# Kernel optimization log

Hardware: AMD Instinct MI355X
Metric: run time of the kernel (lower is better)

The kernel has to match this reference:

```python
import jax, jax.numpy as jnp
import numpy as np

EPS = 1e-5
PC_LO = jnp.array([-51.2, -51.2, -5.0], dtype=jnp.float32)
PC_HI = jnp.array([51.2, 51.2, 3.0], dtype=jnp.float32)
IMG_H, IMG_W = 256, 704
G, P = 1, 4  # num_groups, num_points


def _conv3x3(x, w, b):
    # x: NHWC, w: HWIO
    y = jax.lax.conv_general_dilated(x, w, (1, 1), 'SAME',
                                     dimension_numbers=('NHWC', 'HWIO', 'NHWC'))
    return y + b


def _inorm(x, eps=1e-5):
    # InstanceNorm2d (no affine), stats over H,W per (b,c); x NHWC
    m = jnp.mean(x, axis=(1, 2), keepdims=True)
    v = jnp.var(x, axis=(1, 2), keepdims=True)
    return (x - m) * jax.lax.rsqrt(v + eps)


def _bilinear(img, grid):
    # img [Hf,Wf,C], grid [...,2] in [-1,1]; align_corners=False, zero padding
    Hf, Wf, _ = img.shape
    x = (grid[..., 0] + 1.0) * 0.5 * Wf - 0.5
    y = (grid[..., 1] + 1.0) * 0.5 * Hf - 0.5
    x0 = jnp.floor(x)
    y0 = jnp.floor(y)

    def gather(xi, yi):
        inb = (xi >= 0) & (xi <= Wf - 1) & (yi >= 0) & (yi <= Hf - 1)
        v = img[jnp.clip(yi, 0, Hf - 1).astype(jnp.int32),
                jnp.clip(xi, 0, Wf - 1).astype(jnp.int32)]
        return v * inb[..., None].astype(img.dtype)

    wx1 = x - x0
    wy1 = y - y0
    wx0 = 1.0 - wx1
    wy0 = 1.0 - wy1
    return (gather(x0, y0) * (wx0 * wy0)[..., None]
            + gather(x0 + 1.0, y0) * (wx1 * wy0)[..., None]
            + gather(x0, y0 + 1.0) * (wx0 * wy1)[..., None]
            + gather(x0 + 1.0, y0 + 1.0) * (wx1 * wy1)[..., None])


def setup_inputs() -> dict:
    key = jax.random.key(0)
    ks = jax.random.split(key, 12)
    b, n, C = 1, 6, 128
    Hf, Wf = 32, 88
    Hb, Wb = 128, 128
    return {
        'mlvl_feats': jax.random.normal(ks[0], (b * n, C, Hf, Wf), jnp.float32),
        'lidar2img': jax.random.normal(ks[1], (b, n, 4, 4), jnp.float32),
        'bev_query': jax.random.normal(ks[2], (b, C, Hb, Wb), jnp.float32),
        'bev_pos': jax.random.uniform(ks[3], (b, Hb, Wb, 3), jnp.float32),
        'in_conv_w': jax.random.normal(ks[4], (3, 3, C, C), jnp.float32) * 0.02,
        'in_conv_b': jnp.zeros((C,), jnp.float32),
        'off_w': jax.random.normal(ks[5], (G * P * 3, C), jnp.float32) * 0.02,
        'off_b': jax.random.normal(ks[6], (G * P * 3,), jnp.float32),
        'mid_w1': jax.random.normal(ks[7], (512, 128 * P), jnp.float32) * 0.02,
        'mid_b1': jnp.zeros((512,), jnp.float32),
        'mid_w2': jax.random.normal(ks[8], (512, 512), jnp.float32) * 0.02,
        'mid_b2': jnp.zeros((512,), jnp.float32),
        'mid_w3': jax.random.normal(ks[9], (C, 512), jnp.float32) * 0.02,
        'mid_b3': jnp.zeros((C,), jnp.float32),
        'out_conv_w': jax.random.normal(ks[10], (3, 3, C, C), jnp.float32) * 0.02,
        'out_conv_b': jnp.zeros((C,), jnp.float32),
    }


def reference(mlvl_feats, lidar2img, bev_query, bev_pos, in_conv_w, in_conv_b,
              off_w, off_b, mid_w1, mid_b1, mid_w2, mid_b2, mid_w3, mid_b3,
              out_conv_w, out_conv_b):
    b, C, Hb, Wb = bev_query.shape
    n = lidar2img.shape[1]
    Q = Hb * Wb

    q = jnp.transpose(bev_query, (0, 2, 3, 1))  # NHWC [b,Hb,Wb,C]
    q = q + _conv3x3(q, in_conv_w, in_conv_b)
    q = _inorm(q)

    # --- SegSampling: predict offsets (1x1 conv + sigmoid), build 3D points ---
    off = jax.nn.sigmoid(jnp.einsum('bhwc,oc->bhwo', q, off_w) + off_b)
    off = off.reshape(b, Q, G, P, 3)  # 'b (g p d) h w -> b (h w) g p d'
    off_xy = off[..., :2] * (0.25 + EPS) * 2.0 - (0.25 + EPS)
    off_z = off[..., 2:3] * (4.0 + EPS) * 2.0 - (4.0 + EPS)
    ref = bev_pos.reshape(b, Q, 1, 1, 3) * (PC_HI - PC_LO) + PC_LO
    pts = ref + jnp.concatenate([off_xy, off_z], axis=-1)  # [b,Q,G,P,3]

    # --- project into each camera (sampling_4d) ---
    pts_h = jnp.concatenate([pts, jnp.ones_like(pts[..., :1])], axis=-1)
    cam = jnp.einsum('bnij,bqgpj->bnqgpi', lidar2img, pts_h)  # [b,n,Q,G,P,4]
    homo = cam[..., 2:3]
    uv = cam[..., :2] / jnp.maximum(homo, EPS)
    uv = uv / jnp.array([IMG_W, IMG_H], jnp.float32)  # normalized [0,1]
    valid = ((homo > EPS)
             & (uv[..., 0:1] > 0.0) & (uv[..., 0:1] < 1.0)
             & (uv[..., 1:2] > 0.0) & (uv[..., 1:2] < 1.0)).astype(q.dtype)
    grid = uv * 2.0 - 1.0  # [-1,1] for grid_sample

    # feats: [(b n), C, h, w] -> [b*n, h, w, C] (g=1)
    feat = jnp.transpose(mlvl_feats, (0, 2, 3, 1))
    grid_bn = grid.reshape(b * n, Q * G * P, 2)
    sampled = jax.vmap(_bilinear)(feat, grid_bn)  # [b*n, Q*G*P, C]
    sampled = sampled.reshape(b, n, Q, G, P, C)
    sampled = jnp.sum(sampled * valid, axis=1)  # mask-weighted sum over cameras

    # --- mid_conv: 1x1 conv MLP on (g p c) channels ---
    x = sampled.reshape(b, Hb, Wb, G * P * C)
    x = jax.nn.gelu(jnp.einsum('bhwi,oi->bhwo', x, mid_w1) + mid_b1, approximate=False)
    x = jax.nn.gelu(jnp.einsum('bhwi,oi->bhwo', x, mid_w2) + mid_b2, approximate=False)
    x = jnp.einsum('bhwi,oi->bhwo', x, mid_w3) + mid_b3
    q = _inorm(q + x)
    q = _inorm(q + _conv3x3(q, out_conv_w, out_conv_b))
    return jnp.transpose(q, (0, 3, 1, 2))  # back to NCHW
```

## Files before the change

kernel.cpp:

```cpp
#include <hip/hip_runtime.h>
#include <math.h>

#define QPIX 16384

typedef __bf16 bf16x8 __attribute__((ext_vector_type(8)));
typedef float f32x4 __attribute__((ext_vector_type(4)));

__device__ __forceinline__ unsigned short f2b(float f) {
  unsigned int x = __float_as_uint(f);
  unsigned int r = (x + 0x7fff + ((x >> 16) & 1)) >> 16;
  return (unsigned short)r;
}
__device__ __forceinline__ float b2f(unsigned short u) {
  return __uint_as_float(((unsigned int)u) << 16);
}

__device__ __forceinline__ void gld_lds16(const void* g, void* l) {
  __builtin_amdgcn_global_load_lds((__attribute__((address_space(1))) void*)(g),
                                   (__attribute__((address_space(3))) void*)(l), 16, 0, 0);
}

__device__ __forceinline__ int swz(int row, int ebase) {
  return row * 64 + ((((ebase) >> 3) ^ (row & 7)) << 3);
}

__global__ __launch_bounds__(256) void k_cvt_all(
    const float* __restrict__ feats, const float* __restrict__ bevq,
    const float* __restrict__ w1, const float* __restrict__ w2,
    const float* __restrict__ w3, const float* __restrict__ wo,
    const float* __restrict__ wi, unsigned short* __restrict__ featTb,
    unsigned short* __restrict__ qhi, unsigned short* __restrict__ qlo,
    unsigned short* __restrict__ w1b, unsigned short* __restrict__ w2b,
    unsigned short* __restrict__ w3b, unsigned short* __restrict__ wob,
    unsigned short* __restrict__ wibh, unsigned short* __restrict__ wibl,
    float* __restrict__ zerof) {
  __shared__ float tile[128][33];
  const int b = blockIdx.x, t = threadIdx.x;
  if (b == 0 && t < 160) zerof[t] = 0.f;
  if (b < 528) {
    const int img = b / 88;
    const int pb = (b - img * 88) * 32;
    const int p = t & 31, cg = t >> 5;
#pragma unroll
    for (int ci = 0; ci < 16; ++ci) {
      const int c = cg * 16 + ci;
      tile[c][p] = feats[((size_t)img * 128 + c) * 2816 + pb + p];
    }
    __syncthreads();
    const int c2 = t & 127, pw = t >> 7;
#pragma unroll
    for (int pp = pw; pp < 32; pp += 2)
      featTb[(size_t)img * 2816 * 128 + (size_t)(pb + pp) * 128 + c2] = f2b(tile[c2][pp]);
  } else if (b < 1040) {
    const int pb = (b - 528) * 32;
    const int p = t & 31, cg = t >> 5;
#pragma unroll
    for (int ci = 0; ci < 16; ++ci) {
      const int c = cg * 16 + ci;
      tile[c][p] = bevq[(size_t)c * QPIX + pb + p];
    }
    __syncthreads();
    const int c2 = t & 127, pw = t >> 7;
#pragma unroll
    for (int pp = pw; pp < 32; pp += 2) {
      float v = tile[c2][pp];
      unsigned short h = f2b(v);
      qhi[(size_t)(pb + pp) * 128 + c2] = h;
      qlo[(size_t)(pb + pp) * 128 + c2] = f2b(v - b2f(h));
    }
  } else {
    const int bb = b - 1040;
    if (bb < 1024) {
      int i = bb * 256 + t;
      w1b[i] = f2b(w1[i]);
    } else if (bb < 2048) {
      int i = (bb - 1024) * 256 + t;
      w2b[i] = f2b(w2[i]);
    } else if (bb < 2304) {
      int i = (bb - 2048) * 256 + t;
      w3b[i] = f2b(w3[i]);
    } else if (bb < 2880) {
      int i = (bb - 2304) * 256 + t;
      int n = i & 127, kk = i >> 7;
      int tap = kk >> 7, ci = kk & 127;
      wob[(size_t)n * 1152 + kk] = f2b(wo[(size_t)tap * 16384 + ci * 128 + n]);
    } else {
      int i = (bb - 2880) * 256 + t;
      int n = i & 127, kk = i >> 7;
      int tap = kk >> 7, ci = kk & 127;
      float v = wi[(size_t)tap * 16384 + ci * 128 + n];
      unsigned short h = f2b(v);
      wibh[(size_t)n * 1152 + kk] = h;
      wibl[(size_t)n * 1152 + kk] = f2b(v - b2f(h));
    }
  }
}

template <int BM, int BN, int MODE, int ACT, int RES, int OBF, int STATS>
__global__ __launch_bounds__(256) void mfma_gemm(
    const unsigned short* __restrict__ A, const unsigned short* __restrict__ A2,
    const unsigned short* __restrict__ Wt, const unsigned short* __restrict__ Wt2,
    const float* __restrict__ bias, const float* __restrict__ resid,
    const float* __restrict__ mrres, void* __restrict__ Out,
    float* __restrict__ partial, int N, int K,
    const unsigned short* __restrict__ zbuf) {
  constexpr int MI = BM / 32;
  constexpr int NJ = BN / 32;
  __shared__ unsigned short As[BM * 64];
  __shared__ unsigned short Bs[BN * 64];
  __shared__ unsigned short As2[(MODE == 2) ? BM * 64 : 1];
  __shared__ unsigned short Bs2[(MODE == 2) ? BN * 64 : 1];
  __shared__ float sred[STATS ? (BM / 8) : 1][STATS ? BN : 1];
  __shared__ float ssred[STATS ? (BM / 8) : 1][STATS ? BN : 1];

  const int t = threadIdx.x;
  const int lane = t & 63, w = t >> 6;
  const int wr = w >> 1, wc = w & 1;
  const int n0 = blockIdx.x * BN;
  const int m0 = blockIdx.y * BM;

  const int lrow = lane >> 3;
  const int akk = (((lane & 7) ^ (lrow & 7))) * 8;
  const int arow_l = wr * (BM / 2) + (lane & 15);
  const int brow_l = wc * (BN / 2) + (lane & 15);
  const int klane = (lane >> 4) * 8;

  f32x4 acc[MI][NJ];
#pragma unroll
  for (int i = 0; i < MI; ++i)
#pragma unroll
    for (int j = 0; j < NJ; ++j) acc[i][j] = (f32x4){0.f, 0.f, 0.f, 0.f};

  for (int k0 = 0; k0 < K; k0 += 64) {
#pragma unroll
    for (int q = 0; q < BM / 32; ++q) {
      const int r0 = w * (BM / 4) + q * 8;
      const int arow = r0 + lrow;
      const unsigned short* asrc;
      const unsigned short* asrc2 = zbuf;
      if (MODE == 0) {
        asrc = A + (size_t)(m0 + arow) * K + k0 + akk;
      } else {
        const int tap = k0 >> 7;
        const int dy = tap / 3 - 1, dx = tap % 3 - 1;
        const int pix = m0 + arow;
        const int hs = (pix >> 7) + dy;
        const int xs = (pix & 127) + dx;
        const bool ok = (hs >= 0) && (hs < 128) && (xs >= 0) && (xs < 128);
        const size_t srcoff = (size_t)((hs << 7) | (xs & 127)) * 128 + (k0 & 127) + akk;
        asrc = ok ? A + srcoff : zbuf;
        if (MODE == 2) asrc2 = ok ? A2 + srcoff : zbuf;
      }
      gld_lds16(asrc, &As[r0 * 64]);
      if (MODE == 2) gld_lds16(asrc2, &As2[r0 * 64]);
    }
#pragma unroll
    for (int q = 0; q < BN / 32; ++q) {
      const int r0 = w * (BN / 4) + q * 8;
      const int brow = r0 + lrow;
      gld_lds16(Wt + (size_t)(n0 + brow) * K + k0 + akk, &Bs[r0 * 64]);
      if (MODE == 2)
        gld_lds16(Wt2 + (size_t)(n0 + brow) * K + k0 + akk, &Bs2[r0 * 64]);
    }
    __syncthreads();
#pragma unroll
    for (int ks = 0; ks < 64; ks += 32) {
      bf16x8 af[MI], bfv[NJ];
#pragma unroll
      for (int i = 0; i < MI; ++i)
        af[i] = *(const bf16x8*)&As[swz(arow_l + i * 16, ks + klane)];
#pragma unroll
      for (int j = 0; j < NJ; ++j)
        bfv[j] = *(const bf16x8*)&Bs[swz(brow_l + j * 16, ks + klane)];
#pragma unroll
      for (int i = 0; i < MI; ++i)
#pragma unroll
        for (int j = 0; j < NJ; ++j)
          acc[i][j] = __builtin_amdgcn_mfma_f32_16x16x32_bf16(af[i], bfv[j], acc[i][j], 0, 0, 0);
      if (MODE == 2) {
        bf16x8 af2[MI], bf2[NJ];
#pragma unroll
        for (int i = 0; i < MI; ++i)
          af2[i] = *(const bf16x8*)&As2[swz(arow_l + i * 16, ks + klane)];
#pragma unroll
        for (int j = 0; j < NJ; ++j)
          bf2[j] = *(const bf16x8*)&Bs2[swz(brow_l + j * 16, ks + klane)];
#pragma unroll
        for (int i = 0; i < MI; ++i)
#pragma unroll
          for (int j = 0; j < NJ; ++j) {
            acc[i][j] = __builtin_amdgcn_mfma_f32_16x16x32_bf16(af[i], bf2[j], acc[i][j], 0, 0, 0);
            acc[i][j] = __builtin_amdgcn_mfma_f32_16x16x32_bf16(af2[i], bfv[j], acc[i][j], 0, 0, 0);
          }
      }
    }
    __syncthreads();
  }
  float sj[NJ], ssj[NJ];
#pragma unroll
  for (int j = 0; j < NJ; ++j) { sj[j] = 0.f; ssj[j] = 0.f; }
#pragma unroll
  for (int i = 0; i < MI; ++i) {
    const int mrow = m0 + wr * (BM / 2) + i * 16 + (lane >> 4) * 4;
#pragma unroll
    for (int j = 0; j < NJ; ++j) {
      const int col = n0 + wc * (BN / 2) + j * 16 + (lane & 15);
      const float bz = bias[col];
#pragma unroll
      for (int r = 0; r < 4; ++r) {
        const int m = mrow + r;
        float v = acc[i][j][r] + bz;
        if (RES == 1) v += resid[(size_t)m * 128 + col];
        if (RES == 2) v += resid[(size_t)col * QPIX + m];
        if (RES == 3)
          v += (resid[(size_t)m * 128 + col] - mrres[col]) * mrres[128 + col];
        if (ACT == 1) v = 0.5f * v * (1.f + erff(v * 0.70710678118654752f));
        if (OBF)
          ((unsigned short*)Out)[(size_t)m * N + col] = f2b(v);
        else
          ((float*)Out)[(size_t)m * N + col] = v;
        if (STATS) {
          sj[j] += v;
          ssj[j] += v * v;
        }
      }
    }
  }
  if (STATS) {
    const int cidx = wr * 4 + (lane >> 4);
#pragma unroll
    for (int j = 0; j < NJ; ++j) {
      const int cl = wc * (BN / 2) + j * 16 + (lane & 15);
      sred[cidx][cl] = sj[j];
      ssred[cidx][cl] = ssj[j];
    }
    __syncthreads();
    if (t < BN) {
      float s = 0.f, ss = 0.f;
#pragma unroll
      for (int kk = 0; kk < BM / 8; ++kk) {
        s += sred[kk][t];
        ss += ssred[kk][t];
      }
      partial[(size_t)(n0 + t) * 256 + blockIdx.y] = s;
      partial[32768 + (size_t)(n0 + t) * 256 + blockIdx.y] = ss;
    }
  }
}

__global__ __launch_bounds__(256) void k_stats_final(const float* __restrict__ partial,
                                                     float* __restrict__ mr) {
  __shared__ float s1[256], s2[256];
  const int c = blockIdx.x;
  const int t = threadIdx.x;
  s1[t] = partial[(size_t)c * 256 + t];
  s2[t] = partial[32768 + (size_t)c * 256 + t];
  __syncthreads();
#pragma unroll
  for (int off = 128; off > 0; off >>= 1) {
    if (t < off) {
      s1[t] += s1[t + off];
      s2[t] += s2[t + off];
    }
    __syncthreads();
  }
  if (t == 0) {
    float m = s1[0] * (1.f / 16384.f);
    float var = s2[0] * (1.f / 16384.f) - m * m;
    mr[c] = m;
    mr[128 + c] = rsqrtf(var + 1e-5f);
  }
}

__global__ __launch_bounds__(256) void k_offsets(
    const float* __restrict__ tB, const float* __restrict__ mr,
    const float* __restrict__ offw, const float* __restrict__ offb,
    const float* __restrict__ bpos, const float* __restrict__ l2i,
    float* __restrict__ pw, int* __restrict__ pidx) {
  __shared__ float ldsq[128 * 130];
  __shared__ float wT[128 * 12];
  __shared__ float bl[12];
  __shared__ float ml[128], rl[128];
  __shared__ float offl[128 * 12];
  __shared__ float Ll[96];
  const int t = threadIdx.x;
  const int qb = blockIdx.x * 128;
  for (int i = t; i < 1536; i += 256) wT[(i & 127) * 12 + (i >> 7)] = offw[i];
  if (t < 12) bl[t] = offb[t];
  if (t < 96) Ll[t] = l2i[t];
  if (t < 128) {
    ml[t] = mr[t];
    rl[t] = mr[128 + t];
  }
  __syncthreads();
#pragma unroll
  for (int j = 0; j < 32; ++j) {
    const int e = j * 512 + t * 2;
    const int c0 = e & 127;
    float2 v = *(const float2*)&tB[(size_t)qb * 128 + e];
    v.x = (v.x - ml[c0]) * rl[c0];
    v.y = (v.y - ml[c0 + 1]) * rl[c0 + 1];
    *(float2*)&ldsq[(e >> 7) * 130 + c0] = v;
  }
  __syncthreads();
  {
    const int qlc = t & 127, oh = t >> 7;
    float acc6[6];
#pragma unroll
    for (int o = 0; o < 6; ++o) acc6[o] = bl[oh * 6 + o];
    for (int c = 0; c < 128; ++c) {
      float qv = ldsq[qlc * 130 + c];
#pragma unroll
      for (int o = 0; o < 6; ++o) acc6[o] += qv * wT[c * 12 + oh * 6 + o];
    }
#pragma unroll
    for (int o = 0; o < 6; ++o)
      offl[qlc * 12 + oh * 6 + o] = 1.f / (1.f + expf(-acc6[o]));
  }
  __syncthreads();
  const float EPSf = 1e-5f;
#pragma unroll
  for (int ii = 0; ii < 12; ++ii) {
    const int item = ii * 256 + t;
    const int ql = item / 24;
    const int j = item - ql * 24;
    const int p = j / 6, n = j - p * 6;
    const int q = qb + ql;
    float o0 = offl[ql * 12 + p * 3 + 0];
    float o1 = offl[ql * 12 + p * 3 + 1];
    float o2 = offl[ql * 12 + p * 3 + 2];
    float ox = o0 * ((0.25f + EPSf) * 2.f) - (0.25f + EPSf);
    float oy = o1 * ((0.25f + EPSf) * 2.f) - (0.25f + EPSf);
    float oz = o2 * ((4.f + EPSf) * 2.f) - (4.f + EPSf);
    float px = bpos[q * 3 + 0] * 102.4f - 51.2f + ox;
    float py = bpos[q * 3 + 1] * 102.4f - 51.2f + oy;
    float pz = bpos[q * 3 + 2] * 8.f - 5.f + oz;
    const float* L = Ll + n * 16;
    float c0 = L[0] * px + L[1] * py + L[2] * pz + L[3];
    float c1 = L[4] * px + L[5] * py + L[6] * pz + L[7];
    float c2 = L[8] * px + L[9] * py + L[10] * pz + L[11];
    float d = fmaxf(c2, EPSf);
    float u = (c0 / d) / 704.f;
    float v = (c1 / d) / 256.f;
    float valid = (c2 > EPSf && u > 0.f && u < 1.f && v > 0.f && v < 1.f) ? 1.f : 0.f;
    float x = u * 88.f - 0.5f;
    float y = v * 32.f - 0.5f;
    float x0 = floorf(x), y0 = floorf(y);
    float wx1 = x - x0, wy1 = y - y0;
    float wx0 = 1.f - wx1, wy0 = 1.f - wy1;
    float4 wv;
    int4 iv;
    float* wvp = (float*)&wv;
    int* ivp = (int*)&iv;
#pragma unroll
    for (int k = 0; k < 4; ++k) {
      float xf = x0 + (float)(k & 1);
      float yf = y0 + (float)(k >> 1);
      bool inb = (xf >= 0.f) && (xf <= 87.f) && (yf >= 0.f) && (yf <= 31.f);
      float xc = fminf(fmaxf(xf, 0.f), 87.f);
      float yc = fminf(fmaxf(yf, 0.f), 31.f);
      ivp[k] = ((n * 32 + (int)yc) * 88 + (int)xc) * 128;
      float wgt = ((k & 1) ? wx1 : wx0) * ((k >> 1) ? wy1 : wy0);
      wvp[k] = inb ? wgt * valid : 0.f;
    }
    const size_t gi = (size_t)qb * 24 + item;
    *(float4*)&pw[gi * 4] = wv;
    *(int4*)&pidx[gi * 4] = iv;
  }
}

__global__ __launch_bounds__(256) void k_gather(const float* __restrict__ pw,
                                                const int* __restrict__ pidx,
                                                const unsigned short* __restrict__ featT,
                                                unsigned short* __restrict__ sampled) {
  const int q = blockIdx.x;
  const int t = threadIdx.x;
  const int p = t >> 6;
  const int lane = t & 63;
  const int half = lane >> 5, quad = lane & 31;
  float s0 = 0.f, s1 = 0.f, s2 = 0.f, s3 = 0.f;
#pragma unroll
  for (int cc = 0; cc < 3; ++cc) {
    const int n = half * 3 + cc;
    const size_t e = (size_t)(q * 24 + p * 6 + n) * 4;
    const float4 wv = *(const float4*)&pw[e];
    if (wv.x + wv.y + wv.z + wv.w != 0.f) {
      const int4 iv = *(const int4*)&pidx[e];
      ushort4 v0 = *(const ushort4*)&featT[(size_t)iv.x + quad * 4];
      ushort4 v1 = *(const ushort4*)&featT[(size_t)iv.y + quad * 4];
      ushort4 v2 = *(const ushort4*)&featT[(size_t)iv.z + quad * 4];
      ushort4 v3 = *(const ushort4*)&featT[(size_t)iv.w + quad * 4];
      s0 += wv.x * b2f(v0.x) + wv.y * b2f(v1.x) + wv.z * b2f(v2.x) + wv.w * b2f(v3.x);
      s1 += wv.x * b2f(v0.y) + wv.y * b2f(v1.y) + wv.z * b2f(v2.y) + wv.w * b2f(v3.y);
      s2 += wv.x * b2f(v0.z) + wv.y * b2f(v1.z) + wv.z * b2f(v2.z) + wv.w * b2f(v3.z);
      s3 += wv.x * b2f(v0.w) + wv.y * b2f(v1.w) + wv.z * b2f(v2.w) + wv.w * b2f(v3.w);
    }
  }
  s0 += __shfl_xor(s0, 32);
  s1 += __shfl_xor(s1, 32);
  s2 += __shfl_xor(s2, 32);
  s3 += __shfl_xor(s3, 32);
  if (half == 0) {
    ushort4 o;
    o.x = f2b(s0);
    o.y = f2b(s1);
    o.z = f2b(s2);
    o.w = f2b(s3);
    *(ushort4*)&sampled[(size_t)q * 512 + p * 128 + quad * 4] = o;
  }
}

__global__ __launch_bounds__(256) void k_apply2(const float* __restrict__ a,
                                                const float* __restrict__ mr,
                                                unsigned short* __restrict__ outb) {
  const size_t i = (size_t)blockIdx.x * 256 + threadIdx.x;
  const int c = (int)(i & 127);
  outb[i] = f2b((a[i] - mr[c]) * mr[128 + c]);
}

__global__ __launch_bounds__(256) void k_apply_t(const float* __restrict__ a,
                                                 const float* __restrict__ mr,
                                                 float* __restrict__ out) {
  __shared__ float tile[128][33];
  __shared__ float ml[128], rl[128];
  const int t = threadIdx.x;
  const int pb = blockIdx.x * 32;
  if (t < 128) {
    ml[t] = mr[t];
    rl[t] = mr[128 + t];
  }
  __syncthreads();
#pragma unroll
  for (int j = 0; j < 16; ++j) {
    const int e = j * 256 + t;
    const int pl = e >> 7, c = e & 127;
    const size_t gi = (size_t)(pb + pl) * 128 + c;
    tile[c][pl] = (a[gi] - ml[c]) * rl[c];
  }
  __syncthreads();
  const int p = t & 31, cb = t >> 5;
#pragma unroll
  for (int j = 0; j < 16; ++j) {
    const int c = cb + j * 8;
    out[(size_t)c * QPIX + pb + p] = tile[c][p];
  }
}

extern "C" void kernel_launch(void* const* d_in, const int* in_sizes, int n_in,
                              void* d_out, int out_size, void* d_ws, size_t ws_size,
                              hipStream_t stream) {
  const float* feats = (const float*)d_in[0];
  const float* l2i   = (const float*)d_in[1];
  const float* bevq  = (const float*)d_in[2];
  const float* bpos  = (const float*)d_in[3];
  const float* w_in  = (const float*)d_in[4];
  const float* b_in  = (const float*)d_in[5];
  const float* offw  = (const float*)d_in[6];
  const float* offb  = (const float*)d_in[7];
  const float* w1    = (const float*)d_in[8];
  const float* b1    = (const float*)d_in[9];
  const float* w2    = (const float*)d_in[10];
  const float* b2    = (const float*)d_in[11];
  const float* w3    = (const float*)d_in[12];
  const float* b3    = (const float*)d_in[13];
  const float* w_out = (const float*)d_in[14];
  const float* b_out = (const float*)d_in[15];
  float* out = (float*)d_out;

  const size_t QC = (size_t)QPIX * 128;
  float* ws = (float*)d_ws;
  float* tA = ws;
  float* tBb = tA + QC;
  float* partial = tBb + QC;
  float* mr1 = partial + 65536;
  float* mr2 = mr1 + 256;
  float* mr3 = mr2 + 256;
  float* zerof = mr3 + 256;
  float* pw = zerof + 160;
  int* pidx = (int*)(pw + 1572864);
  unsigned short* us = (unsigned short*)(pidx + 1572864);
  unsigned short* S1b = us;
  unsigned short* S2b = S1b + 8388608;
  unsigned short* featTb = S2b + 8388608;
  unsigned short* qhi = featTb + 2162688;
  unsigned short* qlo = qhi + 2097152;
  unsigned short* w1b = qlo + 2097152;
  unsigned short* w2b = w1b + 262144;
  unsigned short* w3b = w2b + 262144;
  unsigned short* wob = w3b + 65536;
  unsigned short* wibh = wob + 147456;
  unsigned short* wibl = wibh + 147456;
  const unsigned short* zb = (const unsigned short*)zerof;

  dim3 blk(256);

  k_cvt_all<<<4496, blk, 0, stream>>>(feats, bevq, w1, w2, w3, w_out, w_in,
                                      featTb, qhi, qlo, w1b, w2b, w3b, wob, wibh,
                                      wibl, zerof);

  mfma_gemm<64, 64, 2, 0, 2, 0, 1><<<dim3(2, 256), blk, 0, stream>>>(
      qhi, qlo, wibh, wibl, b_in, bevq, nullptr, tA, partial, 128, 1152, zb);
  k_stats_final<<<128, blk, 0, stream>>>(partial, mr1);

  k_offsets<<<128, blk, 0, stream>>>(tA, mr1, offw, offb, bpos, l2i, pw, pidx);

  k_gather<<<QPIX, blk, 0, stream>>>(pw, pidx, featTb, S1b);

  mfma_gemm<128, 128, 0, 1, 0, 1, 0><<<dim3(4, 128), blk, 0, stream>>>(
      S1b, nullptr, w1b, nullptr, b1, nullptr, nullptr, S2b, nullptr, 512, 512, zb);
  mfma_gemm<128, 128, 0, 1, 0, 1, 0><<<dim3(4, 128), blk, 0, stream>>>(
      S2b, nullptr, w2b, nullptr, b2, nullptr, nullptr, S1b, nullptr, 512, 512, zb);
  mfma_gemm<64, 64, 0, 0, 3, 0, 1><<<dim3(2, 256), blk, 0, stream>>>(
      S1b, nullptr, w3b, nullptr, b3, tA, mr1, tBb, partial, 128, 512, zb);
  k_stats_final<<<128, blk, 0, stream>>>(partial, mr2);
  k_apply2<<<8192, blk, 0, stream>>>(tBb, mr2, qhi);

  mfma_gemm<64, 64, 1, 0, 3, 0, 1><<<dim3(2, 256), blk, 0, stream>>>(
      qhi, nullptr, wob, nullptr, b_out, tBb, mr2, tA, partial, 128, 1152, zb);
  k_stats_final<<<128, blk, 0, stream>>>(partial, mr3);
  k_apply_t<<<512, blk, 0, stream>>>(tA, mr3, out);
}
```

Baseline: 161.6 us.

## Fuse stats finalization into GEMMs and merge offset and gather kernels

Removes the three separate stats-final kernels by having the last GEMM block (detected via an atomic counter) reduce the per-block partial sums and write the mean and rstd. Merges the offset computation and the bilinear gather into one kernel that keeps weights and indices in LDS, so the pw/pidx buffers no longer round-trip through global memory. The gather now uses 16-byte loads per lane, and k_apply2 is vectorized to float4. This cuts launches and global traffic, at the cost of a serial 256-row reduction in one block and reliance on counters being zeroed every call.

Result: slower. 347.7 us (+115.2%).

```diff
diff --git a/kernel.cpp b/kernel.cpp
--- a/kernel.cpp
+++ b/kernel.cpp
@@ -5,6 +5,7 @@
 
 typedef __bf16 bf16x8 __attribute__((ext_vector_type(8)));
 typedef float f32x4 __attribute__((ext_vector_type(4)));
+typedef unsigned short ushort8v __attribute__((ext_vector_type(8)));
 
 __device__ __forceinline__ unsigned short f2b(float f) {
   unsigned int x = __float_as_uint(f);
@@ -36,7 +37,7 @@
     float* __restrict__ zerof) {
   __shared__ float tile[128][33];
   const int b = blockIdx.x, t = threadIdx.x;
-  if (b == 0 && t < 160) zerof[t] = 0.f;
+  if (b == 0 && t < 176) zerof[t] = 0.f;
   if (b < 528) {
     const int img = b / 88;
     const int pb = (b - img * 88) * 32;
@@ -102,7 +103,8 @@
     const unsigned short* __restrict__ Wt, const unsigned short* __restrict__ Wt2,
     const float* __restrict__ bias, const float* __restrict__ resid,
     const float* __restrict__ mrres, void* __restrict__ Out,
-    float* __restrict__ partial, int N, int K,
+    float* __restrict__ partial, unsigned* __restrict__ cnt,
+    float* __restrict__ mrout, int N, int K,
     const unsigned short* __restrict__ zbuf) {
   constexpr int MI = BM / 32;
   constexpr int NJ = BN / 32;
@@ -112,6 +114,7 @@
   __shared__ unsigned short Bs2[(MODE == 2) ? BN * 64 : 1];
   __shared__ float sred[STATS ? (BM / 8) : 1][STATS ? BN : 1];
   __shared__ float ssred[STATS ? (BM / 8) : 1][STATS ? BN : 1];
+  __shared__ unsigned lastv;
 
   const int t = threadIdx.x;
   const int lane = t & 63, w = t >> 6;
@@ -242,49 +245,47 @@
         s += sred[kk][t];
         ss += ssred[kk][t];
       }
-      partial[(size_t)(n0 + t) * 256 + blockIdx.y] = s;
-      partial[32768 + (size_t)(n0 + t) * 256 + blockIdx.y] = ss;
-    }
-  }
-}
-
-__global__ __launch_bounds__(256) void k_stats_final(const float* __restrict__ partial,
-                                                     float* __restrict__ mr) {
-  __shared__ float s1[256], s2[256];
-  const int c = blockIdx.x;
-  const int t = threadIdx.x;
-  s1[t] = partial[(size_t)c * 256 + t];
-  s2[t] = partial[32768 + (size_t)c * 256 + t];
-  __syncthreads();
-#pragma unroll
-  for (int off = 128; off > 0; off >>= 1) {
-    if (t < off) {
-      s1[t] += s1[t + off];
-      s2[t] += s2[t + off];
-    }
-    __syncthreads();
-  }
-  if (t == 0) {
-    float m = s1[0] * (1.f / 16384.f);
-    float var = s2[0] * (1.f / 16384.f) - m * m;
-    mr[c] = m;
-    mr[128 + c] = rsqrtf(var + 1e-5f);
-  }
-}
-
-__global__ __launch_bounds__(256) void k_offsets(
+      partial[(size_t)blockIdx.y * 128 + n0 + t] = s;
+      partial[32768 + (size_t)blockIdx.y * 128 + n0 + t] = ss;
+    }
+    __threadfence();
+    __syncthreads();
+    if (t == 0) lastv = atomicAdd(cnt, 1u);
+    __syncthreads();
+    if (lastv == gridDim.x * gridDim.y - 1) {
+      __threadfence();
+      if (t < 128) {
+        float s = 0.f, ss = 0.f;
+#pragma unroll 4
+        for (int y = 0; y < 256; ++y) {
+          s += partial[(size_t)y * 128 + t];
+          ss += partial[32768 + (size_t)y * 128 + t];
+        }
+        float m = s * (1.f / 16384.f);
+        float var = ss * (1.f / 16384.f) - m * m;
+        mrout[t] = m;
+        mrout[128 + t] = rsqrtf(var + 1e-5f);
+      }
+    }
+  }
+}
+
+__global__ __launch_bounds__(256) void k_offgather(
     const float* __restrict__ tB, const float* __restrict__ mr,
     const float* __restrict__ offw, const float* __restrict__ offb,
     const float* __restrict__ bpos, const float* __restrict__ l2i,
-    float* __restrict__ pw, int* __restrict__ pidx) {
-  __shared__ float ldsq[128 * 130];
+    const unsigned short* __restrict__ featT,
+    unsigned short* __restrict__ sampled) {
   __shared__ float wT[128 * 12];
   __shared__ float bl[12];
+  __shared__ float Ll[96];
   __shared__ float ml[128], rl[128];
-  __shared__ float offl[128 * 12];
-  __shared__ float Ll[96];
+  __shared__ float ldsq[16 * 130];
+  __shared__ float offl[16 * 12];
+  __shared__ float cw[16 * 24 * 4];
+  __shared__ int cidx[16 * 24 * 4];
   const int t = threadIdx.x;
-  const int qb = blockIdx.x * 128;
+  const int qb = blockIdx.x * 16;
   for (int i = t; i < 1536; i += 256) wT[(i & 127) * 12 + (i >> 7)] = offw[i];
   if (t < 12) bl[t] = offb[t];
   if (t < 96) Ll[t] = l2i[t];
@@ -292,130 +293,106 @@
     ml[t] = mr[t];
     rl[t] = mr[128 + t];
   }
-  __syncthreads();
-#pragma unroll
-  for (int j = 0; j < 32; ++j) {
-    const int e = j * 512 + t * 2;
-    const int c0 = e & 127;
-    float2 v = *(const float2*)&tB[(size_t)qb * 128 + e];
-    v.x = (v.x - ml[c0]) * rl[c0];
-    v.y = (v.y - ml[c0 + 1]) * rl[c0 + 1];
-    *(float2*)&ldsq[(e >> 7) * 130 + c0] = v;
-  }
+  float4 ra = *(const float4*)&tB[(size_t)qb * 128 + t * 8];
+  float4 rb = *(const float4*)&tB[(size_t)qb * 128 + t * 8 + 4];
   __syncthreads();
   {
-    const int qlc = t & 127, oh = t >> 7;
-    float acc6[6];
-#pragma unroll
-    for (int o = 0; o < 6; ++o) acc6[o] = bl[oh * 6 + o];
-    for (int c = 0; c < 128; ++c) {
-      float qv = ldsq[qlc * 130 + c];
-#pragma unroll
-      for (int o = 0; o < 6; ++o) acc6[o] += qv * wT[c * 12 + oh * 6 + o];
-    }
-#pragma unroll
-    for (int o = 0; o < 6; ++o)
-      offl[qlc * 12 + oh * 6 + o] = 1.f / (1.f + expf(-acc6[o]));
+    const int e = t * 8;
+    const int q = e >> 7, c0 = e & 127;
+    float* d = &ldsq[q * 130 + c0];
+    const float va[8] = {ra.x, ra.y, ra.z, ra.w, rb.x, rb.y, rb.z, rb.w};
+#pragma unroll
+    for (int u = 0; u < 8; ++u) d[u] = (va[u] - ml[c0 + u]) * rl[c0 + u];
+  }
+  __syncthreads();
+  if (t < 192) {
+    const int q = t / 12, o = t - (t / 12) * 12;
+    float acc = bl[o];
+    for (int c = 0; c < 128; ++c) acc += ldsq[q * 130 + c] * wT[c * 12 + o];
+    offl[q * 12 + o] = 1.f / (1.f + expf(-acc));
   }
   __syncthreads();
   const float EPSf = 1e-5f;
 #pragma unroll
-  for (int ii = 0; ii < 12; ++ii) {
+  for (int ii = 0; ii < 2; ++ii) {
     const int item = ii * 256 + t;
-    const int ql = item / 24;
-    const int j = item - ql * 24;
-    const int p = j / 6, n = j - p * 6;
-    const int q = qb + ql;
-    float o0 = offl[ql * 12 + p * 3 + 0];
-    float o1 = offl[ql * 12 + p * 3 + 1];
-    float o2 = offl[ql * 12 + p * 3 + 2];
-    float ox = o0 * ((0.25f + EPSf) * 2.f) - (0.25f + EPSf);
-    float oy = o1 * ((0.25f + EPSf) * 2.f) - (0.25f + EPSf);
-    float oz = o2 * ((4.f + EPSf) * 2.f) - (4.f + EPSf);
-    float px = bpos[q * 3 + 0] * 102.4f - 51.2f + ox;
-    float py = bpos[q * 3 + 1] * 102.4f - 51.2f + oy;
-    float pz = bpos[q * 3 + 2] * 8.f - 5.f + oz;
-    const float* L = Ll + n * 16;
-    float c0 = L[0] * px + L[1] * py + L[2] * pz + L[3];
-    float c1 = L[4] * px + L[5] * py + L[6] * pz + L[7];
-    float c2 = L[8] * px + L[9] * py + L[10] * pz + L[11];
-    float d = fmaxf(c2, EPSf);
-    float u = (c0 / d) / 704.f;
-    float v = (c1 / d) / 256.f;
-    float valid = (c2 > EPSf && u > 0.f && u < 1.f && v > 0.f && v < 1.f) ? 1.f : 0.f;
-    float x = u * 88.f - 0.5f;
-    float y = v * 32.f - 0.5f;
-    float x0 = floorf(x), y0 = floorf(y);
-    float wx1 = x - x0, wy1 = y - y0;
-    float wx0 = 1.f - wx1, wy0 = 1.f - wy1;
-    float4 wv;
-    int4 iv;
-    float* wvp = (float*)&wv;
-    int* ivp = (int*)&iv;
-#pragma unroll
-    for (int k = 0; k < 4; ++k) {
-      float xf = x0 + (float)(k & 1);
-      float yf = y0 + (float)(k >> 1);
-      bool inb = (xf >= 0.f) && (xf <= 87.f) && (yf >= 0.f) && (yf <= 31.f);
-      float xc = fminf(fmaxf(xf, 0.f), 87.f);
-      float yc = fminf(fmaxf(yf, 0.f), 31.f);
-      ivp[k] = ((n * 32 + (int)yc) * 88 + (int)xc) * 128;
-      float wgt = ((k & 1) ? wx1 : wx0) * ((k >> 1) ? wy1 : wy0);
-      wvp[k] = inb ? wgt * valid : 0.f;
-    }
-    const size_t gi = (size_t)qb * 24 + item;
-    *(float4*)&pw[gi * 4] = wv;
-    *(int4*)&pidx[gi * 4] = iv;
-  }
-}
-
-__global__ __launch_bounds__(256) void k_gather(const float* __restrict__ pw,
-                                                const int* __restrict__ pidx,
-                                                const unsigned short* __restrict__ featT,
-                                                unsigned short* __restrict__ sampled) {
-  const int q = blockIdx.x;
-  const int t = threadIdx.x;
-  const int p = t >> 6;
-  const int lane = t & 63;
-  const int half = lane >> 5, quad = lane & 31;
-  float s0 = 0.f, s1 = 0.f, s2 = 0.f, s3 = 0.f;
-#pragma unroll
-  for (int cc = 0; cc < 3; ++cc) {
-    const int n = half * 3 + cc;
-    const size_t e = (size_t)(q * 24 + p * 6 + n) * 4;
-    const float4 wv = *(const float4*)&pw[e];
-    if (wv.x + wv.y + wv.z + wv.w != 0.f) {
-      const int4 iv = *(const int4*)&pidx[e];
-      ushort4 v0 = *(const ushort4*)&featT[(size_t)iv.x + quad * 4];
-      ushort4 v1 = *(const ushort4*)&featT[(size_t)iv.y + quad * 4];
-      ushort4 v2 = *(const ushort4*)&featT[(size_t)iv.z + quad * 4];
-      ushort4 v3 = *(const ushort4*)&featT[(size_t)iv.w + quad * 4];
-      s0 += wv.x * b2f(v0.x) + wv.y * b2f(v1.x) + wv.z * b2f(v2.x) + wv.w * b2f(v3.x);
-      s1 += wv.x * b2f(v0.y) + wv.y * b2f(v1.y) + wv.z * b2f(v2.y) + wv.w * b2f(v3.y);
-      s2 += wv.x * b2f(v0.z) + wv.y * b2f(v1.z) + wv.z * b2f(v2.z) + wv.w * b2f(v3.z);
-      s3 += wv.x * b2f(v0.w) + wv.y * b2f(v1.w) + wv.z * b2f(v2.w) + wv.w * b2f(v3.w);
-    }
-  }
-  s0 += __shfl_xor(s0, 32);
-  s1 += __shfl_xor(s1, 32);
-  s2 += __shfl_xor(s2, 32);
-  s3 += __shfl_xor(s3, 32);
-  if (half == 0) {
-    ushort4 o;
-    o.x = f2b(s0);
-    o.y = f2b(s1);
-    o.z = f2b(s2);
-    o.w = f2b(s3);
-    *(ushort4*)&sampled[(size_t)q * 512 + p * 128 + quad * 4] = o;
+    if (item < 384) {
+      const int ql = item / 24;
+      const int j = item - ql * 24;
+      const int p = j / 6, n = j - p * 6;
+      const int q = qb + ql;
+      float o0 = offl[ql * 12 + p * 3 + 0];
+      float o1 = offl[ql * 12 + p * 3 + 1];
+      float o2 = offl[ql * 12 + p * 3 + 2];
+      float ox = o0 * ((0.25f + EPSf) * 2.f) - (0.25f + EPSf);
+      float oy = o1 * ((0.25f + EPSf) * 2.f) - (0.25f + EPSf);
+      float oz = o2 * ((4.f + EPSf) * 2.f) - (4.f + EPSf);
+      float px = bpos[q * 3 + 0] * 102.4f - 51.2f + ox;
+      float py = bpos[q * 3 + 1] * 102.4f - 51.2f + oy;
+      float pz = bpos[q * 3 + 2] * 8.f - 5.f + oz;
+      const float* L = Ll + n * 16;
+      float c0 = L[0] * px + L[1] * py + L[2] * pz + L[3];
+      float c1 = L[4] * px + L[5] * py + L[6] * pz + L[7];
+      float c2 = L[8] * px + L[9] * py + L[10] * pz + L[11];
+      float d = fmaxf(c2, EPSf);
+      float u = (c0 / d) / 704.f;
+      float v = (c1 / d) / 256.f;
+      float valid = (c2 > EPSf && u > 0.f && u < 1.f && v > 0.f && v < 1.f) ? 1.f : 0.f;
+      float x = u * 88.f - 0.5f;
+      float y = v * 32.f - 0.5f;
+      float x0 = floorf(x), y0 = floorf(y);
+      float wx1 = x - x0, wy1 = y - y0;
+      float wx0 = 1.f - wx1, wy0 = 1.f - wy1;
+#pragma unroll
+      for (int k = 0; k < 4; ++k) {
+        float xf = x0 + (float)(k & 1);
+        float yf = y0 + (float)(k >> 1);
+        bool inb = (xf >= 0.f) && (xf <= 87.f) && (yf >= 0.f) && (yf <= 31.f);
+        float xc = fminf(fmaxf(xf, 0.f), 87.f);
+        float yc = fminf(fmaxf(yf, 0.f), 31.f);
+        cidx[ql * 96 + j * 4 + k] = ((n * 32 + (int)yc) * 88 + (int)xc) * 128;
+        float wgt = ((k & 1) ? wx1 : wx0) * ((k >> 1) ? wy1 : wy0);
+        cw[ql * 96 + j * 4 + k] = inb ? wgt * valid : 0.f;
+      }
+    }
+  }
+  __syncthreads();
+  const int e8 = (t & 15) * 8;
+#pragma unroll
+  for (int rep = 0; rep < 4; ++rep) {
+    const int unit = rep * 16 + (t >> 4);
+    const int q = unit >> 2, p = unit & 3;
+    float s[8] = {0.f, 0.f, 0.f, 0.f, 0.f, 0.f, 0.f, 0.f};
+    const float* cwp = &cw[q * 96 + p * 24];
+    const int* cip = &cidx[q * 96 + p * 24];
+#pragma unroll
+    for (int cc = 0; cc < 24; ++cc) {
+      const float wv = cwp[cc];
+      if (wv != 0.f) {
+        ushort8v v = *(const ushort8v*)&featT[(size_t)cip[cc] + e8];
+#pragma unroll
+        for (int u = 0; u < 8; ++u) s[u] += wv * b2f(v[u]);
+      }
+    }
+    ushort8v o8;
+#pragma unroll
+    for (int u = 0; u < 8; ++u) o8[u] = f2b(s[u]);
+    *(ushort8v*)&sampled[(size_t)(qb + q) * 512 + p * 128 + e8] = o8;
   }
 }
 
 __global__ __launch_bounds__(256) void k_apply2(const float* __restrict__ a,
                                                 const float* __restrict__ mr,
                                                 unsigned short* __restrict__ outb) {
-  const size_t i = (size_t)blockIdx.x * 256 + threadIdx.x;
+  const size_t i = ((size_t)blockIdx.x * 256 + threadIdx.x) * 4;
   const int c = (int)(i & 127);
-  outb[i] = f2b((a[i] - mr[c]) * mr[128 + c]);
+  float4 v = *(const float4*)&a[i];
+  ushort4 o;
+  o.x = f2b((v.x - mr[c]) * mr[128 + c]);
+  o.y = f2b((v.y - mr[c + 1]) * mr[128 + c + 1]);
+  o.z = f2b((v.z - mr[c + 2]) * mr[128 + c + 2]);
+  o.w = f2b((v.w - mr[c + 3]) * mr[128 + c + 3]);
+  *(ushort4*)&outb[i] = o;
 }
 
 __global__ __launch_bounds__(256) void k_apply_t(const float* __restrict__ a,
@@ -476,9 +453,8 @@
   float* mr2 = mr1 + 256;
   float* mr3 = mr2 + 256;
   float* zerof = mr3 + 256;
-  float* pw = zerof + 160;
-  int* pidx = (int*)(pw + 1572864);
-  unsigned short* us = (unsigned short*)(pidx + 1572864);
+  unsigned* cnts = (unsigned*)(zerof + 160);
+  unsigned short* us = (unsigned short*)(zerof + 176);
   unsigned short* S1b = us;
   unsigned short* S2b = S1b + 8388608;
   unsigned short* featTb = S2b + 8388608;
@@ -499,24 +475,24 @@
                                       wibl, zerof);
 
   mfma_gemm<64, 64, 2, 0, 2, 0, 1><<<dim3(2, 256), blk, 0, stream>>>(
-      qhi, qlo, wibh, wibl, b_in, bevq, nullptr, tA, partial, 128, 1152, zb);
-  k_stats_final<<<128, blk, 0, stream>>>(partial, mr1);
-
-  k_offsets<<<128, blk, 0, stream>>>(tA, mr1, offw, offb, bpos, l2i, pw, pidx);
-
-  k_gather<<<QPIX, blk, 0, stream>>>(pw, pidx, featTb, S1b);
+      qhi, qlo, wibh, wibl, b_in, bevq, nullptr, tA, partial, &cnts[0], mr1,
+      128, 1152, zb);
+
+  k_offgather<<<1024, blk, 0, stream>>>(tA, mr1, offw, offb, bpos, l2i, featTb, S1b);
 
   mfma_gemm<128, 128, 0, 1, 0, 1, 0><<<dim3(4, 128), blk, 0, stream>>>(
-      S1b, nullptr, w1b, nullptr, b1, nullptr, nullptr, S2b, nullptr, 512, 512, zb);
+      S1b, nullptr, w1b, nullptr, b1, nullptr, nullptr, S2b, nullptr, nullptr,
+      nullptr, 512, 512, zb);
   mfma_gemm<128, 128, 0, 1, 0, 1, 0><<<dim3(4, 128), blk, 0, stream>>>(
-      S2b, nullptr, w2b, nullptr, b2, nullptr, nullptr, S1b, nullptr, 512, 512, zb);
+      S2b, nullptr, w2b, nullptr, b2, nullptr, nullptr, S1b, nullptr, nullptr,
+      nullptr, 512, 512, zb);
   mfma_gemm<64, 64, 0, 0, 3, 0, 1><<<dim3(2, 256), blk, 0, stream>>>(
-      S1b, nullptr, w3b, nullptr, b3, tA, mr1, tBb, partial, 128, 512, zb);
-  k_stats_final<<<128, blk, 0, stream>>>(partial, mr2);
-  k_apply2<<<8192, blk, 0, stream>>>(tBb, mr2, qhi);
+      S1b, nullptr, w3b, nullptr, b3, tA, mr1, tBb, partial, &cnts[1], mr2,
+      128, 512, zb);
+  k_apply2<<<2048, blk, 0, stream>>>(tBb, mr2, qhi);
 
   mfma_gemm<64, 64, 1, 0, 3, 0, 1><<<dim3(2, 256), blk, 0, stream>>>(
-      qhi, nullptr, wob, nullptr, b_out, tBb, mr2, tA, partial, 128, 1152, zb);
-  k_stats_final<<<128, blk, 0, stream>>>(partial, mr3);
+      qhi, nullptr, wob, nullptr, b_out, tBb, mr2, tA, partial, &cnts[2], mr3,
+      128, 1152, zb);
   k_apply_t<<<512, blk, 0, stream>>>(tA, mr3, out);
 }
```
